# Kernel optimization log

Hardware: AMD Instinct MI355X
Metric: run time of the kernel (lower is better)

Reference implementation:

```python
import jax, jax.numpy as jnp
import numpy as np

B, S, I, H = 64, 512, 512, 512


def setup_inputs() -> dict:
    key = jax.random.key(0)
    ks = jax.random.split(key, 5)
    scale = 1.0 / np.sqrt(I + H)  # keep gates out of hard saturation
    return {
        "x": jax.random.normal(ks[0], (B, S, I), dtype=jnp.float32),
        "h": jax.random.normal(ks[1], (B, H), dtype=jnp.float32),
        "W_r": jax.random.normal(ks[2], (H, I + H), dtype=jnp.float32) * scale,
        "b_r": jnp.zeros((H,), dtype=jnp.float32),
        "W_z": jax.random.normal(ks[3], (H, I + H), dtype=jnp.float32) * scale,
        "b_z": jnp.zeros((H,), dtype=jnp.float32),
        "W_h": jax.random.normal(ks[4], (H, I + H), dtype=jnp.float32) * scale,
        "b_h": jnp.zeros((H,), dtype=jnp.float32),
    }


def reference(x, h, W_r, b_r, W_z, b_z, W_h, b_h):
    # Split each [H, I+H] weight into input part and hidden part (torch cat order: [x, h]).
    i = x.shape[-1]
    Wr_x, Wr_h = W_r[:, :i], W_r[:, i:]
    Wz_x, Wz_h = W_z[:, :i], W_z[:, i:]
    Wh_x, Wh_h = W_h[:, :i], W_h[:, i:]

    # Precompute the input contributions for all timesteps in one big GEMM each.
    xr = jnp.einsum("bsi,hi->bsh", x, Wr_x) + b_r  # [B,S,H]
    xz = jnp.einsum("bsi,hi->bsh", x, Wz_x) + b_z
    xh = jnp.einsum("bsi,hi->bsh", x, Wh_x) + b_h

    def step(h, inp):
        xr_t, xz_t, xh_t = inp  # each [B,H]
        r = jax.nn.sigmoid(xr_t + h @ Wr_h.T)
        z = jax.nn.sigmoid(xz_t + h @ Wz_h.T)
        h_tilde = jnp.tanh(xh_t + (r * h) @ Wh_h.T)
        h_new = (1.0 - z) * h + z * h_tilde
        return h_new, h_new

    # time-major for scan
    xs = (xr.transpose(1, 0, 2), xz.transpose(1, 0, 2), xh.transpose(1, 0, 2))
    h_last, ys = jax.lax.scan(step, h, xs)
    y = ys.transpose(1, 0, 2)  # [B,S,H]; dropout p=0 -> identity
    return y, h_last
```

## Files before the change

kernel.cpp:

```cpp
#include <hip/hip_runtime.h>

#define B_ 64
#define S_ 512
#define H_ 512

typedef unsigned short u16;
typedef unsigned int   u32;

typedef __attribute__((ext_vector_type(8))) short    bf16x8;
typedef __attribute__((ext_vector_type(8))) _Float16 f16x8;
typedef __attribute__((ext_vector_type(4))) float    f32x4;
typedef __attribute__((ext_vector_type(2))) _Float16 h2_t;

#define PJ_GATE ((size_t)512 * 64 * 512)

__device__ inline u16 f2bf(float f) {
  u32 u = __builtin_bit_cast(u32, f);
  u32 r = (u + 0x7fffu + ((u >> 16) & 1u)) >> 16;
  return (u16)r;
}
__device__ inline u32 pkbf2(float a, float b) {
  return (u32)f2bf(a) | ((u32)f2bf(b) << 16);
}
__device__ inline u32 pk2h(float a, float b) {
  _Float16 x = (_Float16)a, y = (_Float16)b;
  return (u32)__builtin_bit_cast(u16, x) | ((u32)__builtin_bit_cast(u16, y) << 16);
}
__device__ inline float sigmoidf_(float x) { return 1.f / (1.f + __expf(-x)); }
__device__ inline float tanhf_(float x) {
  float e = __expf(-2.f * fabsf(x));
  float t = (1.f - e) / (1.f + e);
  return copysignf(t, x);
}

__global__ void k_convert_w(const float* __restrict__ Wr, const float* __restrict__ Wz,
                            const float* __restrict__ Wh, uint4* __restrict__ WF) {
  int g = blockIdx.y;
  const float* Ws = (g == 0) ? Wr : ((g == 1) ? Wz : Wh);
  int i = blockIdx.x * 256 + threadIdx.x;
  int lane = i & 63;
  int kt   = (i >> 6) & 15;
  int rt   = i >> 10;
  int row  = rt * 16 + (lane & 15);
  int col  = 512 + kt * 32 + (lane >> 4) * 8;
  const float* src = Ws + (size_t)row * 1024 + col;
  float4 a = *(const float4*)src;
  float4 b = *(const float4*)(src + 4);
  uint4 o;
  o.x = pk2h(a.x, a.y); o.y = pk2h(a.z, a.w);
  o.z = pk2h(b.x, b.y); o.w = pk2h(b.z, b.w);
  WF[((size_t)(g * 32 + rt) * 16 + kt) * 64 + lane] = o;
}

__global__ __launch_bounds__(256) void k_proj_gemm(
    const float* __restrict__ x,
    const float* __restrict__ Wr, const float* __restrict__ Wz, const float* __restrict__ Wh,
    const float* __restrict__ br, const float* __restrict__ bz, const float* __restrict__ bh,
    u16* __restrict__ P)
{
  const int g  = blockIdx.z;
  const int bm = blockIdx.x * 64;
  const int bn = blockIdx.y * 64;
  const float* Ws = (g == 0) ? Wr : ((g == 1) ? Wz : Wh);
  __shared__ __align__(16) u16 As[64][32];
  __shared__ __align__(16) u16 Bs[64][32];
  const int tid  = threadIdx.x;
  const int lane = tid & 63;
  const int wm   = (tid >> 6) >> 1;
  const int wn   = (tid >> 6) & 1;
  const int srow = tid >> 2;
  const int scol = (tid & 3) * 8;

  f32x4 zero4 = {0.f, 0.f, 0.f, 0.f};
  f32x4 acc[2][2];
  acc[0][0] = zero4; acc[0][1] = zero4; acc[1][0] = zero4; acc[1][1] = zero4;

  for (int k0 = 0; k0 < 512; k0 += 32) {
    __syncthreads();
    {
      const float* xs = x + (size_t)(bm + srow) * 512 + k0 + scol;
      float4 a = *(const float4*)xs, b = *(const float4*)(xs + 4);
      uint4 av; av.x = pkbf2(a.x, a.y); av.y = pkbf2(a.z, a.w);
      av.z = pkbf2(b.x, b.y); av.w = pkbf2(b.z, b.w);
      *(uint4*)(&As[srow][scol]) = av;
      const float* wsrc = Ws + (size_t)(bn + srow) * 1024 + k0 + scol;
      float4 c = *(const float4*)wsrc, d = *(const float4*)(wsrc + 4);
      uint4 bv; bv.x = pkbf2(c.x, c.y); bv.y = pkbf2(c.z, c.w);
      bv.z = pkbf2(d.x, d.y); bv.w = pkbf2(d.z, d.w);
      *(uint4*)(&Bs[srow][scol]) = bv;
    }
    __syncthreads();
#pragma unroll
    for (int mi = 0; mi < 2; ++mi) {
      bf16x8 a = *(const bf16x8*)(&As[wm * 32 + mi * 16 + (lane & 15)][(lane >> 4) * 8]);
#pragma unroll
      for (int ni = 0; ni < 2; ++ni) {
        bf16x8 b = *(const bf16x8*)(&Bs[wn * 32 + ni * 16 + (lane & 15)][(lane >> 4) * 8]);
        acc[mi][ni] = __builtin_amdgcn_mfma_f32_16x16x32_bf16(a, b, acc[mi][ni], 0, 0, 0);
      }
    }
  }
  const float* bias = (g == 0) ? br : ((g == 1) ? bz : bh);
#pragma unroll
  for (int mi = 0; mi < 2; ++mi)
#pragma unroll
    for (int ni = 0; ni < 2; ++ni) {
      int col  = bn + wn * 32 + ni * 16 + (lane & 15);
      float bv = bias[col];
#pragma unroll
      for (int r = 0; r < 4; ++r) {
        int row = bm + wm * 32 + mi * 16 + (lane >> 4) * 4 + r;
        int bb = row >> 9, ss = row & 511;
        float v = acc[mi][ni][r] + bv;
        P[((size_t)g * 512 + ss) * (64 * 512) + (size_t)bb * 512 + col] =
            __builtin_bit_cast(u16, (_Float16)v);
      }
    }
}

__device__ inline void cbar(u32* flag) {
  __syncthreads();
  if (threadIdx.x == 0) {
    __hip_atomic_fetch_add(flag, 1u, __ATOMIC_ACQ_REL, __HIP_MEMORY_SCOPE_AGENT);
    while (__hip_atomic_load(flag, __ATOMIC_ACQUIRE, __HIP_MEMORY_SCOPE_AGENT) < 4u) {
      __builtin_amdgcn_s_sleep(2);
    }
  }
  __syncthreads();
}

__global__ __launch_bounds__(512, 2) void k_gru_scan(
    const float* __restrict__ h0,
    const u16*  __restrict__ P,
    const uint4* __restrict__ WF,
    u16* __restrict__ HX,
    u16* __restrict__ RHX,
    u32* __restrict__ flags,
    float* __restrict__ y,
    float* __restrict__ hlast)
{
  const int q = blockIdx.x & 3;
  const int c = blockIdx.x >> 2;
  const int t = threadIdx.x;
  const int w = t >> 6;
  const int l = t & 63;

  __shared__ __align__(16) u16 whlds[8 * 16 * 64 * 8];
  __shared__ __align__(16) u16 hbuf[16 * 520];

  const int rt = q * 8 + w;
  f16x8 wr[16], wz[16];
#pragma unroll
  for (int kt = 0; kt < 16; ++kt) {
    wr[kt] = __builtin_bit_cast(f16x8, WF[((size_t)(0 * 32 + rt) * 16 + kt) * 64 + l]);
    wz[kt] = __builtin_bit_cast(f16x8, WF[((size_t)(1 * 32 + rt) * 16 + kt) * 64 + l]);
    uint4 whv = WF[((size_t)(2 * 32 + rt) * 16 + kt) * 64 + l];
    *(uint4*)&whlds[((w * 16 + kt) * 64 + l) * 8] = whv;
  }

  const int bloc  = l & 15;
  const int bglob = c * 16 + bloc;
  const int j0    = q * 128 + w * 16 + (l >> 4) * 4;
  f32x4 hreg = *(const f32x4*)(h0 + (size_t)bglob * 512 + j0);
  {
    int b = t >> 5, j = (t & 31) * 16;
    const float4* s = (const float4*)(h0 + (size_t)(c * 16 + b) * 512 + j);
    float4 v0 = s[0], v1 = s[1], v2 = s[2], v3 = s[3];
    uint4 o0, o1;
    o0.x = pk2h(v0.x, v0.y); o0.y = pk2h(v0.z, v0.w);
    o0.z = pk2h(v1.x, v1.y); o0.w = pk2h(v1.z, v1.w);
    o1.x = pk2h(v2.x, v2.y); o1.y = pk2h(v2.z, v2.w);
    o1.z = pk2h(v3.x, v3.y); o1.w = pk2h(v3.z, v3.w);
    uint4* d = (uint4*)&hbuf[b * 520 + j];
    d[0] = o0; d[1] = o1;
  }
  __syncthreads();

  u16* HXc  = HX  + (size_t)c * (16 * 512);
  u16* RHXc = RHX + (size_t)c * (16 * 512);
  const int hbase = bloc * 520 + (l >> 4) * 8;

  size_t offp = (size_t)bglob * 512 + j0;
  size_t offy = (size_t)bglob * 262144 + j0;

  for (int ts = 0; ts < S_; ++ts) {
    f32x4 ar = {0.f, 0.f, 0.f, 0.f}, az = {0.f, 0.f, 0.f, 0.f};
#pragma unroll
    for (int kt = 0; kt < 16; ++kt) {
      f16x8 bf = *(const f16x8*)&hbuf[hbase + kt * 32];
      ar = __builtin_amdgcn_mfma_f32_16x16x32_f16(wr[kt], bf, ar, 0, 0, 0);
      az = __builtin_amdgcn_mfma_f32_16x16x32_f16(wz[kt], bf, az, 0, 0, 0);
    }
    uint2 pru = *(const uint2*)(P + offp);
    uint2 pzu = *(const uint2*)(P + PJ_GATE + offp);
    h2_t pr0 = __builtin_bit_cast(h2_t, pru.x), pr1 = __builtin_bit_cast(h2_t, pru.y);
    h2_t pz0 = __builtin_bit_cast(h2_t, pzu.x), pz1 = __builtin_bit_cast(h2_t, pzu.y);
    float rr0 = sigmoidf_(ar[0] + (float)pr0[0]);
    float rr1 = sigmoidf_(ar[1] + (float)pr0[1]);
    float rr2 = sigmoidf_(ar[2] + (float)pr1[0]);
    float rr3 = sigmoidf_(ar[3] + (float)pr1[1]);
    float zz0 = sigmoidf_(az[0] + (float)pz0[0]);
    float zz1 = sigmoidf_(az[1] + (float)pz0[1]);
    float zz2 = sigmoidf_(az[2] + (float)pz1[0]);
    float zz3 = sigmoidf_(az[3] + (float)pz1[1]);
    uint2 rh;
    rh.x = pk2h(rr0 * hreg[0], rr1 * hreg[1]);
    rh.y = pk2h(rr2 * hreg[2], rr3 * hreg[3]);
    *(uint2*)&RHXc[bloc * 512 + j0] = rh;

    cbar(&flags[(ts * 2 + 0) * 4 + c]);

    {
      int b = t >> 5, j = (t & 31) * 16;
      const uint4* s = (const uint4*)&RHXc[b * 512 + j];
      uint4 v0 = s[0], v1 = s[1];
      uint4* d = (uint4*)&hbuf[b * 520 + j];
      d[0] = v0; d[1] = v1;
    }
    __syncthreads();

    f32x4 ah = {0.f, 0.f, 0.f, 0.f};
#pragma unroll
    for (int kt = 0; kt < 16; ++kt) {
      f16x8 bf = *(const f16x8*)&hbuf[hbase + kt * 32];
      f16x8 wh = *(const f16x8*)&whlds[((w * 16 + kt) * 64 + l) * 8];
      ah = __builtin_amdgcn_mfma_f32_16x16x32_f16(wh, bf, ah, 0, 0, 0);
    }
    uint2 phu = *(const uint2*)(P + 2 * PJ_GATE + offp);
    h2_t ph0 = __builtin_bit_cast(h2_t, phu.x), ph1 = __builtin_bit_cast(h2_t, phu.y);
    float ht0 = tanhf_(ah[0] + (float)ph0[0]);
    float ht1 = tanhf_(ah[1] + (float)ph0[1]);
    float ht2 = tanhf_(ah[2] + (float)ph1[0]);
    float ht3 = tanhf_(ah[3] + (float)ph1[1]);
    hreg[0] = zz0 * ht0 + (1.f - zz0) * hreg[0];
    hreg[1] = zz1 * ht1 + (1.f - zz1) * hreg[1];
    hreg[2] = zz2 * ht2 + (1.f - zz2) * hreg[2];
    hreg[3] = zz3 * ht3 + (1.f - zz3) * hreg[3];
    *(f32x4*)(y + offy) = hreg;
    uint2 hx;
    hx.x = pk2h(hreg[0], hreg[1]);
    hx.y = pk2h(hreg[2], hreg[3]);
    *(uint2*)&HXc[bloc * 512 + j0] = hx;

    cbar(&flags[(ts * 2 + 1) * 4 + c]);

    if (ts != S_ - 1) {
      int b = t >> 5, j = (t & 31) * 16;
      const uint4* s = (const uint4*)&HXc[b * 512 + j];
      uint4 v0 = s[0], v1 = s[1];
      uint4* d = (uint4*)&hbuf[b * 520 + j];
      d[0] = v0; d[1] = v1;
      __syncthreads();
    }
    offp += 32768;
    offy += 512;
  }

  *(f32x4*)(hlast + (size_t)bglob * 512 + j0) = hreg;
}

extern "C" void kernel_launch(void* const* d_in, const int* in_sizes, int n_in,
                              void* d_out, int out_size, void* d_ws, size_t ws_size,
                              hipStream_t stream) {
  const float* x  = (const float*)d_in[0];
  const float* h0 = (const float*)d_in[1];
  const float* Wr = (const float*)d_in[2];
  const float* br = (const float*)d_in[3];
  const float* Wz = (const float*)d_in[4];
  const float* bz = (const float*)d_in[5];
  const float* Wh = (const float*)d_in[6];
  const float* bh = (const float*)d_in[7];

  char* ws = (char*)d_ws;
  uint4* WF    = (uint4*)ws;
  u16*   P     = (u16*)(ws + 2097152);
  u16*   HX    = (u16*)(ws + 102760448);
  u16*   RHX   = (u16*)(ws + 102825984);
  u32*   flags = (u32*)(ws + 102891520);

  float* y     = (float*)d_out;
  float* hlast = y + (size_t)B_ * S_ * H_;

  hipMemsetAsync(flags, 0, 512 * 2 * 4 * sizeof(u32), stream);
  k_convert_w<<<dim3(128, 3), dim3(256), 0, stream>>>(Wr, Wz, Wh, WF);
  k_proj_gemm<<<dim3(512, 8, 3), dim3(256), 0, stream>>>(x, Wr, Wz, Wh, br, bz, bh, P);
  k_gru_scan<<<dim3(16), dim3(512), 0, stream>>>(h0, P, WF, HX, RHX, flags, y, hlast);
}
```

Before: 3.264 ms.

## Split W_h GEMM along K across blocks to halve cross-block barriers per step

Each of the four cooperating blocks now computes a K-slice partial of the candidate-gate GEMM over its own r*h columns and publishes fp32 partials plus z. Every block then reduces all partials redundantly and updates the full hidden state locally, so only one inter-block barrier per timestep remains instead of two, and the h exchange through global memory disappears. It also prefetches the next step's gate projections and uses nontemporal stores for y. The cost is redundant reduction work, more global partial-sum traffic, a larger LDS weight buffer, and the full hidden state held in each block.

```diff
diff --git a/kernel.cpp b/kernel.cpp
--- a/kernel.cpp
+++ b/kernel.cpp
@@ -118,23 +118,12 @@
     }
 }
 
-__device__ inline void cbar(u32* flag) {
-  __syncthreads();
-  if (threadIdx.x == 0) {
-    __hip_atomic_fetch_add(flag, 1u, __ATOMIC_ACQ_REL, __HIP_MEMORY_SCOPE_AGENT);
-    while (__hip_atomic_load(flag, __ATOMIC_ACQUIRE, __HIP_MEMORY_SCOPE_AGENT) < 4u) {
-      __builtin_amdgcn_s_sleep(2);
-    }
-  }
-  __syncthreads();
-}
-
 __global__ __launch_bounds__(512, 2) void k_gru_scan(
     const float* __restrict__ h0,
     const u16*  __restrict__ P,
     const uint4* __restrict__ WF,
-    u16* __restrict__ HX,
-    u16* __restrict__ RHX,
+    float* __restrict__ PT,
+    u16* __restrict__ ZX,
     u32* __restrict__ flags,
     float* __restrict__ y,
     float* __restrict__ hlast)
@@ -144,9 +133,13 @@
   const int t = threadIdx.x;
   const int w = t >> 6;
   const int l = t & 63;
-
-  __shared__ __align__(16) u16 whlds[8 * 16 * 64 * 8];
+  const int bq = l & 15;
+  const int g4 = l >> 4;
+  const int bglob = c * 16 + bq;
+
+  __shared__ __align__(16) u16 whlds[32 * 4 * 64 * 8];
   __shared__ __align__(16) u16 hbuf[16 * 520];
+  __shared__ __align__(16) u16 rhbuf[16 * 136];
 
   const int rt = q * 8 + w;
   f16x8 wr[16], wz[16];
@@ -154,109 +147,152 @@
   for (int kt = 0; kt < 16; ++kt) {
     wr[kt] = __builtin_bit_cast(f16x8, WF[((size_t)(0 * 32 + rt) * 16 + kt) * 64 + l]);
     wz[kt] = __builtin_bit_cast(f16x8, WF[((size_t)(1 * 32 + rt) * 16 + kt) * 64 + l]);
-    uint4 whv = WF[((size_t)(2 * 32 + rt) * 16 + kt) * 64 + l];
-    *(uint4*)&whlds[((w * 16 + kt) * 64 + l) * 8] = whv;
-  }
-
-  const int bloc  = l & 15;
-  const int bglob = c * 16 + bloc;
-  const int j0    = q * 128 + w * 16 + (l >> 4) * 4;
-  f32x4 hreg = *(const f32x4*)(h0 + (size_t)bglob * 512 + j0);
-  {
-    int b = t >> 5, j = (t & 31) * 16;
-    const float4* s = (const float4*)(h0 + (size_t)(c * 16 + b) * 512 + j);
-    float4 v0 = s[0], v1 = s[1], v2 = s[2], v3 = s[3];
-    uint4 o0, o1;
-    o0.x = pk2h(v0.x, v0.y); o0.y = pk2h(v0.z, v0.w);
-    o0.z = pk2h(v1.x, v1.y); o0.w = pk2h(v1.z, v1.w);
-    o1.x = pk2h(v2.x, v2.y); o1.y = pk2h(v2.z, v2.w);
-    o1.z = pk2h(v3.x, v3.y); o1.w = pk2h(v3.z, v3.w);
-    uint4* d = (uint4*)&hbuf[b * 520 + j];
-    d[0] = o0; d[1] = o1;
+  }
+#pragma unroll
+  for (int it = 0; it < 16; ++it) {
+    int i = it * 512 + t;
+    int jt = i >> 8, kk = (i >> 6) & 3, ln = i & 63;
+    uint4 v = WF[((size_t)(2 * 32 + jt) * 16 + (q * 4 + kk)) * 64 + ln];
+    *(uint4*)&whlds[((jt * 4 + kk) * 64 + ln) * 8] = v;
+  }
+
+  f32x4 hold[4];
+#pragma unroll
+  for (int jt = 0; jt < 4; ++jt) {
+    int j = w * 64 + jt * 16 + g4 * 4;
+    hold[jt] = *(const f32x4*)(h0 + (size_t)bglob * 512 + j);
+    uint2 hp; hp.x = pk2h(hold[jt][0], hold[jt][1]); hp.y = pk2h(hold[jt][2], hold[jt][3]);
+    *(uint2*)&hbuf[bq * 520 + j] = hp;
   }
   __syncthreads();
 
-  u16* HXc  = HX  + (size_t)c * (16 * 512);
-  u16* RHXc = RHX + (size_t)c * (16 * 512);
-  const int hbase = bloc * 520 + (l >> 4) * 8;
-
-  size_t offp = (size_t)bglob * 512 + j0;
-  size_t offy = (size_t)bglob * 262144 + j0;
+  const int j0A = q * 128 + w * 16 + g4 * 4;
+  const int klA = w * 16 + g4 * 4;
+  const u16* Ppr = P + (size_t)bglob * 512 + j0A;
+  const u16* Ppz = P + PJ_GATE + (size_t)bglob * 512 + j0A;
+
+  const int PT_PAR = 4 * 4 * 16 * 512;
+  const int ZX_PAR = 4 * 16 * 512;
+
+  uint2 pru = *(const uint2*)Ppr;
+  uint2 pzu = *(const uint2*)Ppz;
 
   for (int ts = 0; ts < S_; ++ts) {
+    const int par = ts & 1;
     f32x4 ar = {0.f, 0.f, 0.f, 0.f}, az = {0.f, 0.f, 0.f, 0.f};
 #pragma unroll
     for (int kt = 0; kt < 16; ++kt) {
-      f16x8 bf = *(const f16x8*)&hbuf[hbase + kt * 32];
-      ar = __builtin_amdgcn_mfma_f32_16x16x32_f16(wr[kt], bf, ar, 0, 0, 0);
-      az = __builtin_amdgcn_mfma_f32_16x16x32_f16(wz[kt], bf, az, 0, 0, 0);
-    }
-    uint2 pru = *(const uint2*)(P + offp);
-    uint2 pzu = *(const uint2*)(P + PJ_GATE + offp);
-    h2_t pr0 = __builtin_bit_cast(h2_t, pru.x), pr1 = __builtin_bit_cast(h2_t, pru.y);
-    h2_t pz0 = __builtin_bit_cast(h2_t, pzu.x), pz1 = __builtin_bit_cast(h2_t, pzu.y);
-    float rr0 = sigmoidf_(ar[0] + (float)pr0[0]);
-    float rr1 = sigmoidf_(ar[1] + (float)pr0[1]);
-    float rr2 = sigmoidf_(ar[2] + (float)pr1[0]);
-    float rr3 = sigmoidf_(ar[3] + (float)pr1[1]);
-    float zz0 = sigmoidf_(az[0] + (float)pz0[0]);
-    float zz1 = sigmoidf_(az[1] + (float)pz0[1]);
-    float zz2 = sigmoidf_(az[2] + (float)pz1[0]);
-    float zz3 = sigmoidf_(az[3] + (float)pz1[1]);
-    uint2 rh;
-    rh.x = pk2h(rr0 * hreg[0], rr1 * hreg[1]);
-    rh.y = pk2h(rr2 * hreg[2], rr3 * hreg[3]);
-    *(uint2*)&RHXc[bloc * 512 + j0] = rh;
-
-    cbar(&flags[(ts * 2 + 0) * 4 + c]);
-
+      f16x8 hv = *(const f16x8*)&hbuf[bq * 520 + g4 * 8 + kt * 32];
+      ar = __builtin_amdgcn_mfma_f32_16x16x32_f16(wr[kt], hv, ar, 0, 0, 0);
+      az = __builtin_amdgcn_mfma_f32_16x16x32_f16(wz[kt], hv, az, 0, 0, 0);
+    }
     {
-      int b = t >> 5, j = (t & 31) * 16;
-      const uint4* s = (const uint4*)&RHXc[b * 512 + j];
-      uint4 v0 = s[0], v1 = s[1];
-      uint4* d = (uint4*)&hbuf[b * 520 + j];
-      d[0] = v0; d[1] = v1;
-    }
-    __syncthreads();
-
-    f32x4 ah = {0.f, 0.f, 0.f, 0.f};
-#pragma unroll
-    for (int kt = 0; kt < 16; ++kt) {
-      f16x8 bf = *(const f16x8*)&hbuf[hbase + kt * 32];
-      f16x8 wh = *(const f16x8*)&whlds[((w * 16 + kt) * 64 + l) * 8];
-      ah = __builtin_amdgcn_mfma_f32_16x16x32_f16(wh, bf, ah, 0, 0, 0);
-    }
-    uint2 phu = *(const uint2*)(P + 2 * PJ_GATE + offp);
-    h2_t ph0 = __builtin_bit_cast(h2_t, phu.x), ph1 = __builtin_bit_cast(h2_t, phu.y);
-    float ht0 = tanhf_(ah[0] + (float)ph0[0]);
-    float ht1 = tanhf_(ah[1] + (float)ph0[1]);
-    float ht2 = tanhf_(ah[2] + (float)ph1[0]);
-    float ht3 = tanhf_(ah[3] + (float)ph1[1]);
-    hreg[0] = zz0 * ht0 + (1.f - zz0) * hreg[0];
-    hreg[1] = zz1 * ht1 + (1.f - zz1) * hreg[1];
-    hreg[2] = zz2 * ht2 + (1.f - zz2) * hreg[2];
-    hreg[3] = zz3 * ht3 + (1.f - zz3) * hreg[3];
-    *(f32x4*)(y + offy) = hreg;
-    uint2 hx;
-    hx.x = pk2h(hreg[0], hreg[1]);
-    hx.y = pk2h(hreg[2], hreg[3]);
-    *(uint2*)&HXc[bloc * 512 + j0] = hx;
-
-    cbar(&flags[(ts * 2 + 1) * 4 + c]);
-
-    if (ts != S_ - 1) {
-      int b = t >> 5, j = (t & 31) * 16;
-      const uint4* s = (const uint4*)&HXc[b * 512 + j];
-      uint4 v0 = s[0], v1 = s[1];
-      uint4* d = (uint4*)&hbuf[b * 520 + j];
-      d[0] = v0; d[1] = v1;
-      __syncthreads();
-    }
-    offp += 32768;
-    offy += 512;
-  }
-
-  *(f32x4*)(hlast + (size_t)bglob * 512 + j0) = hreg;
+      h2_t pr0 = __builtin_bit_cast(h2_t, pru.x), pr1 = __builtin_bit_cast(h2_t, pru.y);
+      h2_t pz0 = __builtin_bit_cast(h2_t, pzu.x), pz1 = __builtin_bit_cast(h2_t, pzu.y);
+      float rr0 = sigmoidf_(ar[0] + (float)pr0[0]);
+      float rr1 = sigmoidf_(ar[1] + (float)pr0[1]);
+      float rr2 = sigmoidf_(ar[2] + (float)pr1[0]);
+      float rr3 = sigmoidf_(ar[3] + (float)pr1[1]);
+      float zz0 = sigmoidf_(az[0] + (float)pz0[0]);
+      float zz1 = sigmoidf_(az[1] + (float)pz0[1]);
+      float zz2 = sigmoidf_(az[2] + (float)pz1[0]);
+      float zz3 = sigmoidf_(az[3] + (float)pz1[1]);
+      uint2 hAp = *(const uint2*)&hbuf[bq * 520 + j0A];
+      h2_t hA0 = __builtin_bit_cast(h2_t, hAp.x), hA1 = __builtin_bit_cast(h2_t, hAp.y);
+      uint2 rp;
+      rp.x = pk2h(rr0 * (float)hA0[0], rr1 * (float)hA0[1]);
+      rp.y = pk2h(rr2 * (float)hA1[0], rr3 * (float)hA1[1]);
+      *(uint2*)&rhbuf[bq * 136 + klA] = rp;
+      uint2 zp; zp.x = pk2h(zz0, zz1); zp.y = pk2h(zz2, zz3);
+      *(uint2*)(ZX + par * ZX_PAR + c * (16 * 512) + bq * 512 + j0A) = zp;
+    }
+    __syncthreads();
+
+    f32x4 pb0 = {0.f,0.f,0.f,0.f}, pb1 = pb0, pb2 = pb0, pb3 = pb0;
+#pragma unroll
+    for (int kk = 0; kk < 4; ++kk) {
+      f16x8 rv = *(const f16x8*)&rhbuf[bq * 136 + g4 * 8 + kk * 32];
+      f16x8 w0 = *(const f16x8*)&whlds[(((w * 4 + 0) * 4 + kk) * 64 + l) * 8];
+      f16x8 w1 = *(const f16x8*)&whlds[(((w * 4 + 1) * 4 + kk) * 64 + l) * 8];
+      f16x8 w2 = *(const f16x8*)&whlds[(((w * 4 + 2) * 4 + kk) * 64 + l) * 8];
+      f16x8 w3 = *(const f16x8*)&whlds[(((w * 4 + 3) * 4 + kk) * 64 + l) * 8];
+      pb0 = __builtin_amdgcn_mfma_f32_16x16x32_f16(w0, rv, pb0, 0, 0, 0);
+      pb1 = __builtin_amdgcn_mfma_f32_16x16x32_f16(w1, rv, pb1, 0, 0, 0);
+      pb2 = __builtin_amdgcn_mfma_f32_16x16x32_f16(w2, rv, pb2, 0, 0, 0);
+      pb3 = __builtin_amdgcn_mfma_f32_16x16x32_f16(w3, rv, pb3, 0, 0, 0);
+    }
+    float* PTme = PT + par * PT_PAR + ((c * 4 + q) * 16 + bq) * 512;
+    {
+      int jb = w * 64 + g4 * 4;
+      *(f32x4*)(PTme + jb)      = pb0;
+      *(f32x4*)(PTme + jb + 16) = pb1;
+      *(f32x4*)(PTme + jb + 32) = pb2;
+      *(f32x4*)(PTme + jb + 48) = pb3;
+    }
+    uint2 phv[4];
+#pragma unroll
+    for (int jt = 0; jt < 4; ++jt) {
+      int j = w * 64 + jt * 16 + g4 * 4;
+      phv[jt] = *(const uint2*)(P + 2 * PJ_GATE + ((size_t)ts * 64 + bglob) * 512 + j);
+    }
+
+    __syncthreads();
+    u32* flg = &flags[ts * 4 + c];
+    if (t == 0)
+      __hip_atomic_fetch_add(flg, 1u, __ATOMIC_RELEASE, __HIP_MEMORY_SCOPE_AGENT);
+    while (__hip_atomic_load(flg, __ATOMIC_RELAXED, __HIP_MEMORY_SCOPE_AGENT) < 4u)
+      __builtin_amdgcn_s_sleep(1);
+    (void)__hip_atomic_load(flg, __ATOMIC_ACQUIRE, __HIP_MEMORY_SCOPE_AGENT);
+
+    {
+      int tsn = (ts < S_ - 1) ? ts + 1 : ts;
+      pru = *(const uint2*)(Ppr + (size_t)tsn * 32768);
+      pzu = *(const uint2*)(Ppz + (size_t)tsn * 32768);
+    }
+
+    const float* PTc = PT + par * PT_PAR + (c * 4) * (16 * 512);
+    const u16*   ZXc = ZX + par * ZX_PAR + c * (16 * 512);
+    const bool own = ((w >> 1) == q);
+    f32x4 pbl[4] = {pb0, pb1, pb2, pb3};
+#pragma unroll
+    for (int jt = 0; jt < 4; ++jt) {
+      int j = w * 64 + jt * 16 + g4 * 4;
+      f32x4 s = pbl[jt];
+#pragma unroll
+      for (int p = 0; p < 4; ++p) {
+        if (p == q) continue;
+        s += *(const f32x4*)(PTc + (p * 16 + bq) * 512 + j);
+      }
+      uint2 zv = *(const uint2*)(ZXc + bq * 512 + j);
+      h2_t z0 = __builtin_bit_cast(h2_t, zv.x), z1 = __builtin_bit_cast(h2_t, zv.y);
+      h2_t p0 = __builtin_bit_cast(h2_t, phv[jt].x), p1 = __builtin_bit_cast(h2_t, phv[jt].y);
+      float ht0 = tanhf_(s[0] + (float)p0[0]);
+      float ht1 = tanhf_(s[1] + (float)p0[1]);
+      float ht2 = tanhf_(s[2] + (float)p1[0]);
+      float ht3 = tanhf_(s[3] + (float)p1[1]);
+      float zf0 = (float)z0[0], zf1 = (float)z0[1], zf2 = (float)z1[0], zf3 = (float)z1[1];
+      f32x4 hn;
+      hn[0] = zf0 * ht0 + (1.f - zf0) * hold[jt][0];
+      hn[1] = zf1 * ht1 + (1.f - zf1) * hold[jt][1];
+      hn[2] = zf2 * ht2 + (1.f - zf2) * hold[jt][2];
+      hn[3] = zf3 * ht3 + (1.f - zf3) * hold[jt][3];
+      hold[jt] = hn;
+      uint2 hp; hp.x = pk2h(hn[0], hn[1]); hp.y = pk2h(hn[2], hn[3]);
+      *(uint2*)&hbuf[bq * 520 + j] = hp;
+      if (own)
+        __builtin_nontemporal_store(hn,
+            (f32x4*)(y + (size_t)bglob * 262144 + (size_t)ts * 512 + j));
+    }
+    __syncthreads();
+  }
+
+  if ((w >> 1) == q) {
+#pragma unroll
+    for (int jt = 0; jt < 4; ++jt) {
+      int j = w * 64 + jt * 16 + g4 * 4;
+      *(f32x4*)(hlast + (size_t)bglob * 512 + j) = hold[jt];
+    }
+  }
 }
 
 extern "C" void kernel_launch(void* const* d_in, const int* in_sizes, int n_in,
@@ -274,15 +310,15 @@
   char* ws = (char*)d_ws;
   uint4* WF    = (uint4*)ws;
   u16*   P     = (u16*)(ws + 2097152);
-  u16*   HX    = (u16*)(ws + 102760448);
-  u16*   RHX   = (u16*)(ws + 102825984);
-  u32*   flags = (u32*)(ws + 102891520);
+  float* PT    = (float*)(ws + 102760448);
+  u16*   ZX    = (u16*)(ws + 103809024);
+  u32*   flags = (u32*)(ws + 103940096);
 
   float* y     = (float*)d_out;
   float* hlast = y + (size_t)B_ * S_ * H_;
 
-  hipMemsetAsync(flags, 0, 512 * 2 * 4 * sizeof(u32), stream);
+  hipMemsetAsync(flags, 0, 512 * 4 * sizeof(u32), stream);
   k_convert_w<<<dim3(128, 3), dim3(256), 0, stream>>>(Wr, Wz, Wh, WF);
   k_proj_gemm<<<dim3(512, 8, 3), dim3(256), 0, stream>>>(x, Wr, Wz, Wh, br, bz, bh, P);
-  k_gru_scan<<<dim3(16), dim3(512), 0, stream>>>(h0, P, WF, HX, RHX, flags, y, hlast);
-}
+  k_gru_scan<<<dim3(16), dim3(512), 0, stream>>>(h0, P, WF, PT, ZX, flags, y, hlast);
+}
```

Result: slower. 5.780 ms (+77.1%).

## Replace atomic counter barriers with tagged-data flag exchange between scan blocks

Applied to the files above, without the earlier changes.

Removes the per-step global atomic counter barriers and instead packs each fp16 hidden value with a step tag in a 32-bit word, so consumer blocks spin directly on the data they need, with double-buffered parity slots. Each block keeps its own slice in LDS and pulls only the other three quarters, avoiding a full round-trip through global memory plus barrier. It also moves Wh into registers, prefetches the projection inputs one step ahead, and uses nontemporal stores for y. The trade-offs are more register pressure and many fine-grained relaxed atomic loads and stores.

```diff
diff --git a/kernel.cpp b/kernel.cpp
--- a/kernel.cpp
+++ b/kernel.cpp
@@ -6,6 +6,7 @@
 
 typedef unsigned short u16;
 typedef unsigned int   u32;
+typedef unsigned long long u64;
 
 typedef __attribute__((ext_vector_type(8))) short    bf16x8;
 typedef __attribute__((ext_vector_type(8))) _Float16 f16x8;
@@ -22,15 +23,24 @@
 __device__ inline u32 pkbf2(float a, float b) {
   return (u32)f2bf(a) | ((u32)f2bf(b) << 16);
 }
+__device__ inline u16 f2h(float a) {
+  _Float16 x = (_Float16)a;
+  return __builtin_bit_cast(u16, x);
+}
 __device__ inline u32 pk2h(float a, float b) {
-  _Float16 x = (_Float16)a, y = (_Float16)b;
-  return (u32)__builtin_bit_cast(u16, x) | ((u32)__builtin_bit_cast(u16, y) << 16);
+  return (u32)f2h(a) | ((u32)f2h(b) << 16);
 }
 __device__ inline float sigmoidf_(float x) { return 1.f / (1.f + __expf(-x)); }
 __device__ inline float tanhf_(float x) {
   float e = __expf(-2.f * fabsf(x));
   float t = (1.f - e) / (1.f + e);
   return copysignf(t, x);
+}
+__device__ inline void xstore(u32* p, u32 v) {
+  __hip_atomic_store(p, v, __ATOMIC_RELAXED, __HIP_MEMORY_SCOPE_AGENT);
+}
+__device__ inline u64 xload(const u64* p) {
+  return __hip_atomic_load(p, __ATOMIC_RELAXED, __HIP_MEMORY_SCOPE_AGENT);
 }
 
 __global__ void k_convert_w(const float* __restrict__ Wr, const float* __restrict__ Wz,
@@ -118,24 +128,12 @@
     }
 }
 
-__device__ inline void cbar(u32* flag) {
-  __syncthreads();
-  if (threadIdx.x == 0) {
-    __hip_atomic_fetch_add(flag, 1u, __ATOMIC_ACQ_REL, __HIP_MEMORY_SCOPE_AGENT);
-    while (__hip_atomic_load(flag, __ATOMIC_ACQUIRE, __HIP_MEMORY_SCOPE_AGENT) < 4u) {
-      __builtin_amdgcn_s_sleep(2);
-    }
-  }
-  __syncthreads();
-}
-
 __global__ __launch_bounds__(512, 2) void k_gru_scan(
     const float* __restrict__ h0,
     const u16*  __restrict__ P,
     const uint4* __restrict__ WF,
-    u16* __restrict__ HX,
-    u16* __restrict__ RHX,
-    u32* __restrict__ flags,
+    u32* __restrict__ RHX,
+    u32* __restrict__ HX,
     float* __restrict__ y,
     float* __restrict__ hlast)
 {
@@ -144,24 +142,24 @@
   const int t = threadIdx.x;
   const int w = t >> 6;
   const int l = t & 63;
-
-  __shared__ __align__(16) u16 whlds[8 * 16 * 64 * 8];
+  const int bq = l & 15;
+  const int g4 = l >> 4;
+  const int bglob = c * 16 + bq;
+  const int rt  = q * 8 + w;
+  const int j0A = q * 128 + w * 16 + g4 * 4;
+
   __shared__ __align__(16) u16 hbuf[16 * 520];
-
-  const int rt = q * 8 + w;
-  f16x8 wr[16], wz[16];
+  __shared__ __align__(16) u16 rhbuf[16 * 520];
+
+  f16x8 wr[16], wz[16], wh[16];
 #pragma unroll
   for (int kt = 0; kt < 16; ++kt) {
     wr[kt] = __builtin_bit_cast(f16x8, WF[((size_t)(0 * 32 + rt) * 16 + kt) * 64 + l]);
     wz[kt] = __builtin_bit_cast(f16x8, WF[((size_t)(1 * 32 + rt) * 16 + kt) * 64 + l]);
-    uint4 whv = WF[((size_t)(2 * 32 + rt) * 16 + kt) * 64 + l];
-    *(uint4*)&whlds[((w * 16 + kt) * 64 + l) * 8] = whv;
+    wh[kt] = __builtin_bit_cast(f16x8, WF[((size_t)(2 * 32 + rt) * 16 + kt) * 64 + l]);
   }
 
-  const int bloc  = l & 15;
-  const int bglob = c * 16 + bloc;
-  const int j0    = q * 128 + w * 16 + (l >> 4) * 4;
-  f32x4 hreg = *(const f32x4*)(h0 + (size_t)bglob * 512 + j0);
+  f32x4 hold = *(const f32x4*)(h0 + (size_t)bglob * 512 + j0A);
   {
     int b = t >> 5, j = (t & 31) * 16;
     const float4* s = (const float4*)(h0 + (size_t)(c * 16 + b) * 512 + j);
@@ -176,23 +174,34 @@
   }
   __syncthreads();
 
-  u16* HXc  = HX  + (size_t)c * (16 * 512);
-  u16* RHXc = RHX + (size_t)c * (16 * 512);
-  const int hbase = bloc * 520 + (l >> 4) * 8;
-
-  size_t offp = (size_t)bglob * 512 + j0;
-  size_t offy = (size_t)bglob * 262144 + j0;
+  const u16* Ppr = P + (size_t)bglob * 512 + j0A;
+  const u16* Ppz = P + PJ_GATE + (size_t)bglob * 512 + j0A;
+  const u16* Pph = P + 2 * PJ_GATE + (size_t)bglob * 512 + j0A;
+
+  const int kL = t >> 2;
+  const int b0 = (t & 3) * 4;
+  const int CL = 512 * 16;
+  const int PAR = 4 * CL;
+
+  uint2 pru = *(const uint2*)Ppr;
+  uint2 pzu = *(const uint2*)Ppz;
 
   for (int ts = 0; ts < S_; ++ts) {
+    const int par = ts & 1;
+    const u32 tag = (u32)(ts + 1);
+    const u64 tp  = ((u64)tag << 16) | ((u64)tag << 48);
+    u32* RHXp = RHX + par * PAR + c * CL;
+    u32* HXp  = HX  + par * PAR + c * CL;
+
+    uint2 phu = *(const uint2*)(Pph + (size_t)ts * 32768);
+
     f32x4 ar = {0.f, 0.f, 0.f, 0.f}, az = {0.f, 0.f, 0.f, 0.f};
 #pragma unroll
     for (int kt = 0; kt < 16; ++kt) {
-      f16x8 bf = *(const f16x8*)&hbuf[hbase + kt * 32];
-      ar = __builtin_amdgcn_mfma_f32_16x16x32_f16(wr[kt], bf, ar, 0, 0, 0);
-      az = __builtin_amdgcn_mfma_f32_16x16x32_f16(wz[kt], bf, az, 0, 0, 0);
-    }
-    uint2 pru = *(const uint2*)(P + offp);
-    uint2 pzu = *(const uint2*)(P + PJ_GATE + offp);
+      f16x8 hv = *(const f16x8*)&hbuf[bq * 520 + g4 * 8 + kt * 32];
+      ar = __builtin_amdgcn_mfma_f32_16x16x32_f16(wr[kt], hv, ar, 0, 0, 0);
+      az = __builtin_amdgcn_mfma_f32_16x16x32_f16(wz[kt], hv, az, 0, 0, 0);
+    }
     h2_t pr0 = __builtin_bit_cast(h2_t, pru.x), pr1 = __builtin_bit_cast(h2_t, pru.y);
     h2_t pz0 = __builtin_bit_cast(h2_t, pzu.x), pz1 = __builtin_bit_cast(h2_t, pzu.y);
     float rr0 = sigmoidf_(ar[0] + (float)pr0[0]);
@@ -203,60 +212,92 @@
     float zz1 = sigmoidf_(az[1] + (float)pz0[1]);
     float zz2 = sigmoidf_(az[2] + (float)pz1[0]);
     float zz3 = sigmoidf_(az[3] + (float)pz1[1]);
-    uint2 rh;
-    rh.x = pk2h(rr0 * hreg[0], rr1 * hreg[1]);
-    rh.y = pk2h(rr2 * hreg[2], rr3 * hreg[3]);
-    *(uint2*)&RHXc[bloc * 512 + j0] = rh;
-
-    cbar(&flags[(ts * 2 + 0) * 4 + c]);
-
-    {
-      int b = t >> 5, j = (t & 31) * 16;
-      const uint4* s = (const uint4*)&RHXc[b * 512 + j];
-      uint4 v0 = s[0], v1 = s[1];
-      uint4* d = (uint4*)&hbuf[b * 520 + j];
-      d[0] = v0; d[1] = v1;
+    u16 rh0 = f2h(rr0 * hold[0]), rh1 = f2h(rr1 * hold[1]);
+    u16 rh2 = f2h(rr2 * hold[2]), rh3 = f2h(rr3 * hold[3]);
+    *(uint2*)&rhbuf[bq * 520 + j0A] =
+        uint2{(u32)rh0 | ((u32)rh1 << 16), (u32)rh2 | ((u32)rh3 << 16)};
+    xstore(RHXp + (j0A + 0) * 16 + bq, (tag << 16) | rh0);
+    xstore(RHXp + (j0A + 1) * 16 + bq, (tag << 16) | rh1);
+    xstore(RHXp + (j0A + 2) * 16 + bq, (tag << 16) | rh2);
+    xstore(RHXp + (j0A + 3) * 16 + bq, (tag << 16) | rh3);
+
+#pragma unroll
+    for (int p = 1; p < 4; ++p) {
+      int pq = (q + p) & 3;
+      int kg = pq * 128 + kL;
+      const u64* pa = (const u64*)(RHXp + kg * 16 + b0);
+      u64 A = xload(pa), Bv = xload(pa + 1);
+      while (((A ^ tp) & 0xffff0000ffff0000ull) != 0ull) {
+        __builtin_amdgcn_s_sleep(1);
+        A = xload(pa);
+      }
+      while (((Bv ^ tp) & 0xffff0000ffff0000ull) != 0ull) {
+        __builtin_amdgcn_s_sleep(1);
+        Bv = xload(pa + 1);
+      }
+      rhbuf[(b0 + 0) * 520 + kg] = (u16)A;
+      rhbuf[(b0 + 1) * 520 + kg] = (u16)(A >> 32);
+      rhbuf[(b0 + 2) * 520 + kg] = (u16)Bv;
+      rhbuf[(b0 + 3) * 520 + kg] = (u16)(Bv >> 32);
     }
     __syncthreads();
 
     f32x4 ah = {0.f, 0.f, 0.f, 0.f};
 #pragma unroll
     for (int kt = 0; kt < 16; ++kt) {
-      f16x8 bf = *(const f16x8*)&hbuf[hbase + kt * 32];
-      f16x8 wh = *(const f16x8*)&whlds[((w * 16 + kt) * 64 + l) * 8];
-      ah = __builtin_amdgcn_mfma_f32_16x16x32_f16(wh, bf, ah, 0, 0, 0);
-    }
-    uint2 phu = *(const uint2*)(P + 2 * PJ_GATE + offp);
+      f16x8 rv = *(const f16x8*)&rhbuf[bq * 520 + g4 * 8 + kt * 32];
+      ah = __builtin_amdgcn_mfma_f32_16x16x32_f16(wh[kt], rv, ah, 0, 0, 0);
+    }
     h2_t ph0 = __builtin_bit_cast(h2_t, phu.x), ph1 = __builtin_bit_cast(h2_t, phu.y);
     float ht0 = tanhf_(ah[0] + (float)ph0[0]);
     float ht1 = tanhf_(ah[1] + (float)ph0[1]);
     float ht2 = tanhf_(ah[2] + (float)ph1[0]);
     float ht3 = tanhf_(ah[3] + (float)ph1[1]);
-    hreg[0] = zz0 * ht0 + (1.f - zz0) * hreg[0];
-    hreg[1] = zz1 * ht1 + (1.f - zz1) * hreg[1];
-    hreg[2] = zz2 * ht2 + (1.f - zz2) * hreg[2];
-    hreg[3] = zz3 * ht3 + (1.f - zz3) * hreg[3];
-    *(f32x4*)(y + offy) = hreg;
-    uint2 hx;
-    hx.x = pk2h(hreg[0], hreg[1]);
-    hx.y = pk2h(hreg[2], hreg[3]);
-    *(uint2*)&HXc[bloc * 512 + j0] = hx;
-
-    cbar(&flags[(ts * 2 + 1) * 4 + c]);
-
-    if (ts != S_ - 1) {
-      int b = t >> 5, j = (t & 31) * 16;
-      const uint4* s = (const uint4*)&HXc[b * 512 + j];
-      uint4 v0 = s[0], v1 = s[1];
-      uint4* d = (uint4*)&hbuf[b * 520 + j];
-      d[0] = v0; d[1] = v1;
-      __syncthreads();
-    }
-    offp += 32768;
-    offy += 512;
+    f32x4 hn;
+    hn[0] = zz0 * ht0 + (1.f - zz0) * hold[0];
+    hn[1] = zz1 * ht1 + (1.f - zz1) * hold[1];
+    hn[2] = zz2 * ht2 + (1.f - zz2) * hold[2];
+    hn[3] = zz3 * ht3 + (1.f - zz3) * hold[3];
+    hold = hn;
+    __builtin_nontemporal_store(hn,
+        (f32x4*)(y + (size_t)bglob * 262144 + (size_t)ts * 512 + j0A));
+    u16 h0b = f2h(hn[0]), h1b = f2h(hn[1]), h2b = f2h(hn[2]), h3b = f2h(hn[3]);
+    *(uint2*)&hbuf[bq * 520 + j0A] =
+        uint2{(u32)h0b | ((u32)h1b << 16), (u32)h2b | ((u32)h3b << 16)};
+    xstore(HXp + (j0A + 0) * 16 + bq, (tag << 16) | h0b);
+    xstore(HXp + (j0A + 1) * 16 + bq, (tag << 16) | h1b);
+    xstore(HXp + (j0A + 2) * 16 + bq, (tag << 16) | h2b);
+    xstore(HXp + (j0A + 3) * 16 + bq, (tag << 16) | h3b);
+
+    {
+      int tsn = (ts < S_ - 1) ? ts + 1 : ts;
+      pru = *(const uint2*)(Ppr + (size_t)tsn * 32768);
+      pzu = *(const uint2*)(Ppz + (size_t)tsn * 32768);
+    }
+
+#pragma unroll
+    for (int p = 1; p < 4; ++p) {
+      int pq = (q + p) & 3;
+      int jg = pq * 128 + kL;
+      const u64* pa = (const u64*)(HXp + jg * 16 + b0);
+      u64 A = xload(pa), Bv = xload(pa + 1);
+      while (((A ^ tp) & 0xffff0000ffff0000ull) != 0ull) {
+        __builtin_amdgcn_s_sleep(1);
+        A = xload(pa);
+      }
+      while (((Bv ^ tp) & 0xffff0000ffff0000ull) != 0ull) {
+        __builtin_amdgcn_s_sleep(1);
+        Bv = xload(pa + 1);
+      }
+      hbuf[(b0 + 0) * 520 + jg] = (u16)A;
+      hbuf[(b0 + 1) * 520 + jg] = (u16)(A >> 32);
+      hbuf[(b0 + 2) * 520 + jg] = (u16)Bv;
+      hbuf[(b0 + 3) * 520 + jg] = (u16)(Bv >> 32);
+    }
+    __syncthreads();
   }
 
-  *(f32x4*)(hlast + (size_t)bglob * 512 + j0) = hreg;
+  *(f32x4*)(hlast + (size_t)bglob * 512 + j0A) = hold;
 }
 
 extern "C" void kernel_launch(void* const* d_in, const int* in_sizes, int n_in,
@@ -272,17 +313,16 @@
   const float* bh = (const float*)d_in[7];
 
   char* ws = (char*)d_ws;
-  uint4* WF    = (uint4*)ws;
-  u16*   P     = (u16*)(ws + 2097152);
-  u16*   HX    = (u16*)(ws + 102760448);
-  u16*   RHX   = (u16*)(ws + 102825984);
-  u32*   flags = (u32*)(ws + 102891520);
+  uint4* WF  = (uint4*)ws;
+  u16*   P   = (u16*)(ws + 2097152);
+  u32*   RHX = (u32*)(ws + 102760448);
+  u32*   HX  = (u32*)(ws + 103022592);
 
   float* y     = (float*)d_out;
   float* hlast = y + (size_t)B_ * S_ * H_;
 
-  hipMemsetAsync(flags, 0, 512 * 2 * 4 * sizeof(u32), stream);
+  hipMemsetAsync(ws + 102760448, 0, 524288, stream);
   k_convert_w<<<dim3(128, 3), dim3(256), 0, stream>>>(Wr, Wz, Wh, WF);
   k_proj_gemm<<<dim3(512, 8, 3), dim3(256), 0, stream>>>(x, Wr, Wz, Wh, br, bz, bh, P);
-  k_gru_scan<<<dim3(16), dim3(512), 0, stream>>>(h0, P, WF, HX, RHX, flags, y, hlast);
-}
+  k_gru_scan<<<dim3(16), dim3(512), 0, stream>>>(h0, P, WF, RHX, HX, y, hlast);
+}
```

Result: faster. 3.188 ms (-2.3%).
